# Kernel optimization log

Measured on AMD Instinct MI355X. Metric: run time of the kernel, lower is better.

The kernel has to match this reference:

```python
import jax, jax.numpy as jnp
import numpy as np

# Hardware-emulation constants (from init_kwargs, NeuroSim-style QLinear)
WL_IN = 8        # input activation bit width (bit-serial)
WL_W = 8         # weight bit width
CELL_BIT = 2     # bits per memory cell -> 4 weight slices
SUB = 128        # crossbar sub-array size (rows summed in analog)
ADC_BITS = 5     # ADC precision per partial sum
ONOFF = 10.0     # cell on/off conductance ratio
VARI = 0.05      # multiplicative device variation sigma


def _adc_quant(x, bits, axes):
    # LinearQuantizeOut: uniform quantization between tensor min/max
    mn = jnp.min(x, axis=axes, keepdims=True)
    mx = jnp.max(x, axis=axes, keepdims=True)
    step = (mx - mn) * (2.0 ** (-bits))
    step = jnp.where(step <= 0, 1.0, step)
    idx = jnp.clip(jnp.floor((x - mn) / step), 0.0, 2.0 ** bits - 1.0)
    return idx * step + mn


def _qlinear_hw(x, w, noise):
    """Analog PIM crossbar emulation of y = x @ w.T with bit-serial inputs,
    bit-sliced cells, on/off-ratio offset + dummy column, device variation,
    per-subarray ADC quantization."""
    B, N = x.shape
    F = w.shape[0]
    I, W, K = WL_IN, WL_W, WL_W // CELL_BIT
    cr = 2.0 ** CELL_BIT
    lower, upper = 1.0 / ONOFF, 1.0
    S = (N + SUB - 1) // SUB
    Np = S * SUB
    # quantize input to I bits in [0,1]; weight to W-bit integer in [0, 2^W-1]
    xq = jnp.round(jnp.clip(x, 0.0, 1.0) * (2.0 ** I - 1.0))            # [B, N]
    Xi = jnp.clip(jnp.round((w + 1.0) * 0.5 * (2.0 ** W - 1.0)), 0.0, 2.0 ** W - 1.0)  # [F, N]
    xq = jnp.pad(xq, ((0, 0), (0, Np - N)))
    Xi = jnp.pad(Xi, ((0, 0), (0, Np - N)))
    zpow = 2.0 ** jnp.arange(I, dtype=x.dtype)
    kpow = cr ** jnp.arange(K, dtype=x.dtype)
    bits = jnp.mod(jnp.floor(xq[..., None] / zpow), 2.0)                # [B, Np, I]
    slc = jnp.mod(jnp.floor(Xi[..., None] / kpow), cr)                  # [F, Np, K]
    g = slc * (upper - lower) + (cr - 1.0) * lower                      # cell conductances
    g = g * (1.0 + VARI * noise)                                        # device variation
    bits = bits.reshape(B, S, SUB, I)
    g = g.reshape(F, S, SUB, K)
    # analog partial sums per (input bit i, subarray s, weight slice k)
    P = jnp.einsum('bsai,fsak->iskbf', bits, g)                         # [I,S,K,B,F]
    # dummy column (all cells at lowest conductance), identical across F
    D = jnp.transpose(bits.sum(axis=2), (2, 1, 0)) * ((cr - 1.0) * lower)  # [I,S,B]
    Pq = _adc_quant(P, ADC_BITS, axes=(3, 4))
    Dq = _adc_quant(D, ADC_BITS, axes=(2,))
    scal = (2.0 ** jnp.arange(I, dtype=x.dtype))[:, None] * (cr ** jnp.arange(K, dtype=x.dtype))[None, :]
    acc = jnp.einsum('iskbf,ik->bf', Pq - Dq[:, :, None, :, None], scal) / (upper - lower)
    # undo integer mappings: w = 2*Xi/(2^W-1) - 1, x = xq/(2^I-1)
    out = 2.0 * acc / ((2.0 ** I - 1.0) * (2.0 ** W - 1.0)) \
          - xq.sum(axis=1, keepdims=True) / (2.0 ** I - 1.0)
    return out


def _qlinear(x, w, noise):
    # straight-through quantized weight (WAGE-style STE) + hardware forward
    Xi = jnp.clip(jnp.round((w + 1.0) * 0.5 * (2.0 ** WL_W - 1.0)), 0.0, 2.0 ** WL_W - 1.0)
    wq = 2.0 * Xi / (2.0 ** WL_W - 1.0) - 1.0
    wq_ste = w + jax.lax.stop_gradient(wq - w)
    out_ideal = x @ wq_ste.T
    out_hw = _qlinear_hw(x, w, noise)
    return out_ideal + jax.lax.stop_gradient(out_hw - out_ideal)


def setup_inputs() -> dict:
    key = jax.random.key(0)
    k1, k2, k3, k4, k5 = jax.random.split(key, 5)
    x = jax.random.uniform(k1, (1024, 784), dtype=jnp.float32)
    w1 = jax.random.normal(k2, (512, 784), dtype=jnp.float32) * 0.05
    w3 = jax.random.normal(k3, (10, 512), dtype=jnp.float32) * 0.08
    noise1 = jax.random.normal(k4, (512, 896, 4), dtype=jnp.float32)  # 784 padded to 7*128
    noise3 = jax.random.normal(k5, (10, 512, 4), dtype=jnp.float32)   # 512 = 4*128 exact
    return {"x": x, "w1": w1, "w3": w3, "noise1": noise1, "noise3": noise3}


def reference(x, w1, w3, noise1, noise3):
    h = jnp.tanh(_qlinear(x, w1, noise1))   # QLinear(784,512) + Tanh
    return _qlinear(h, w3, noise3)          # QLinear(512,10)
```

## Files before the change

### kernel.cpp

```cpp
#include <hip/hip_runtime.h>

#define FLTMAX 3.402823466e+38f


__global__ void prep1_kernel(const float* __restrict__ x, float* __restrict__ xq1,
                             float* __restrict__ sx1, unsigned* __restrict__ stats1)
{
    __shared__ float red[128];
    int b = blockIdx.x;
    if (blockIdx.x == 0) {
        for (int t = threadIdx.x; t < 224; t += 128) {
            stats1[t * 2] = 0x7F7FFFFFu; stats1[t * 2 + 1] = 0u;
        }
    }
    float psum = 0.f;
    for (int n = threadIdx.x; n < 896; n += 128) {
        float v = 0.f;
        if (n < 784) {
            float xv = x[b * 784 + n];
            xv = fminf(fmaxf(xv, 0.f), 1.f);
            v = rintf(__fmul_rn(xv, 255.f));
        }
        xq1[b * 896 + n] = v;
        psum += v;
    }
    red[threadIdx.x] = psum;
    __syncthreads();
    for (int w = 64; w >= 1; w >>= 1) {
        if (threadIdx.x < w) red[threadIdx.x] += red[threadIdx.x + w];
        __syncthreads();
    }
    if (threadIdx.x == 0) sx1[b] = red[0];
}

__global__ void bitpack_kernel(const float* __restrict__ xq1, unsigned* __restrict__ xqb)
{
    int gid = blockIdx.x * 256 + threadIdx.x;
    if (gid >= 1024 * 28) return;
    int b = gid / 28, w = gid % 28;
    unsigned words[8] = {0, 0, 0, 0, 0, 0, 0, 0};
    const float* src = &xq1[b * 896 + w * 32];
#pragma unroll 8
    for (int n = 0; n < 32; ++n) {
        int v = (int)src[n];
#pragma unroll
        for (int i = 0; i < 8; ++i) words[i] |= ((unsigned)((v >> i) & 1)) << n;
    }
#pragma unroll
    for (int i = 0; i < 8; ++i) xqb[(i * 1024 + b) * 28 + w] = words[i];
}

__global__ void prepg1t_kernel(const float* __restrict__ w1, const float* __restrict__ noise1,
                               float* __restrict__ g1t)
{
    __shared__ float t[4][32][33];
    const int n0 = blockIdx.x * 32, f0 = blockIdx.y * 32;
    const int tid = threadIdx.x;
    {
        int n = tid & 31, fi = tid >> 5;
#pragma unroll
        for (int p = 0; p < 4; ++p) {
            int f = p * 8 + fi;
            int gn = n0 + n, gf = f0 + f;
            float gv[4] = {0.f, 0.f, 0.f, 0.f};
            if (gn < 784) {
                float w = w1[gf * 784 + gn];
                float Xi = fminf(fmaxf(rintf(__fmul_rn(__fmul_rn(__fadd_rn(w, 1.f), 0.5f), 255.f)),
                                       0.f), 255.f);
                int xi = (int)Xi;
                float4 nz = *(const float4*)&noise1[(gf * 896 + gn) * 4];
                float nzv[4] = {nz.x, nz.y, nz.z, nz.w};
#pragma unroll
                for (int k = 0; k < 4; ++k) {
                    int slc = (xi >> (2 * k)) & 3;
                    float base = __fadd_rn(__fmul_rn((float)slc, 0.9f), 0.3f);
                    float nf = __fadd_rn(1.f, __fmul_rn(0.05f, nzv[k]));
                    gv[k] = __fmul_rn(base, nf);
                }
            }
#pragma unroll
            for (int k = 0; k < 4; ++k) t[k][n][f] = gv[k];
        }
    }
    __syncthreads();
    {
        int f = tid & 31, nn = tid >> 5;
#pragma unroll
        for (int p = 0; p < 4; ++p) {
            int n = p * 8 + nn;
#pragma unroll
            for (int k = 0; k < 4; ++k)
                g1t[(n0 + n) * 2048 + k * 512 + f0 + f] = t[k][n][f];
        }
    }
}

__global__ void prepg2_kernel(const float* __restrict__ w3, const float* __restrict__ noise3,
                              float* __restrict__ g2t)
{
    int gid = blockIdx.x * 256 + threadIdx.x;
    if (gid >= 10 * 512) return;
    int f = gid / 512, n = gid % 512;
    float w = w3[f * 512 + n];
    float Xi = fminf(fmaxf(rintf(__fmul_rn(__fmul_rn(__fadd_rn(w, 1.f), 0.5f), 255.f)),
                           0.f), 255.f);
    int xi = (int)Xi;
#pragma unroll
    for (int k = 0; k < 4; ++k) {
        int slc = (xi >> (2 * k)) & 3;
        float base = __fadd_rn(__fmul_rn((float)slc, 0.9f), 0.3f);
        float nf = __fadd_rn(1.f, __fmul_rn(0.05f, noise3[(f * 512 + n) * 4 + k]));
        g2t[n * 40 + k * 10 + f] = __fmul_rn(base, nf);
    }
}

__global__ void dqpop_kernel(const unsigned* __restrict__ xqb, float* __restrict__ Dq,
                             int S, int wpr)
{
    __shared__ float red[512];
    const int i = blockIdx.x / S, s = blockIdx.x % S;
    const int tid = threadIdx.x;
    float D[4];
    float mn = FLTMAX, mx = -FLTMAX;
#pragma unroll
    for (int u = 0; u < 4; ++u) {
        int b = tid + u * 256;
        uint4 w = *(const uint4*)&xqb[(i * 1024 + b) * wpr + s * 4];
        int c = __popc(w.x) + __popc(w.y) + __popc(w.z) + __popc(w.w);
        D[u] = __fmul_rn((float)c, 0.3f);
        mn = fminf(mn, D[u]);
        mx = fmaxf(mx, D[u]);
    }
    red[tid] = mn; red[256 + tid] = mx;
    __syncthreads();
    for (int w = 128; w >= 1; w >>= 1) {
        if (tid < w) {
            red[tid] = fminf(red[tid], red[tid + w]);
            red[256 + tid] = fmaxf(red[256 + tid], red[256 + tid + w]);
        }
        __syncthreads();
    }
    mn = red[0]; mx = red[256];
    float step = __fmul_rn(__fsub_rn(mx, mn), 0.03125f);
    if (step <= 0.f) step = 1.f;
#pragma unroll
    for (int u = 0; u < 4; ++u) {
        int b = tid + u * 256;
        float idx = fminf(fmaxf(floorf(__fdiv_rn(__fsub_rn(D[u], mn), step)), 0.f), 31.f);
        Dq[(i * S + s) * 1024 + b] = __fadd_rn(__fmul_rn(idx, step), mn);
    }
}

__global__ void dterm_kernel(const float* __restrict__ Dq, float* __restrict__ dterm, int S)
{
    int b = blockIdx.x * 256 + threadIdx.x;
    if (b >= 1024) return;
    float sum = 0.f;
    for (int i = 0; i < 8; ++i) {
        float sc = (float)(85 << i);
        for (int s = 0; s < S; ++s) sum = fmaf(Dq[(i * S + s) * 1024 + b], sc, sum);
    }
    dterm[b] = sum;
}

#define BK 32
__global__ __launch_bounds__(256, 4) void mm1_kernel(
    const unsigned* __restrict__ xqb, const float* __restrict__ g1t,
    float* __restrict__ P, unsigned* __restrict__ stats, int s0)
{
    __shared__ __align__(16) float Bs[BK][132];
    __shared__ unsigned Abits[128];
    __shared__ float red[512];
    const int tid = threadIdx.x;
    const int sl = blockIdx.x >> 6;
    const int r = blockIdx.x & 63;
    const int i = r >> 3;
    const int b0 = (r & 7) * 128;
    const int s = s0 + sl;
    const int colBase = blockIdx.y * 128;
    const int tx = tid & 15, ty = tid >> 4;

    const int aB = tid >> 5;
    const int eB = (tid & 31) << 2;

    float4 pB[4];
    unsigned pAw = 0;
#pragma unroll
    for (int u = 0; u < 4; ++u)
        pB[u] = *(const float4*)&g1t[(s * 128 + u * 8 + aB) * 2048 + colBase + eB];
    if (tid < 128) pAw = xqb[(i * 1024 + b0 + tid) * 28 + s * 4];

    float acc[8][8] = {};

    for (int ac = 0; ac < 4; ++ac) {
        __syncthreads();
#pragma unroll
        for (int u = 0; u < 4; ++u)
            *(float4*)&Bs[u * 8 + aB][eB] = pB[u];
        if (tid < 128) Abits[tid] = pAw;
        __syncthreads();

        if (ac < 3) {
            const int n0 = s * 128 + (ac + 1) * BK;
#pragma unroll
            for (int u = 0; u < 4; ++u)
                pB[u] = *(const float4*)&g1t[(n0 + u * 8 + aB) * 2048 + colBase + eB];
            if (tid < 128) pAw = xqb[(i * 1024 + b0 + tid) * 28 + s * 4 + ac + 1];
        }

        unsigned wrd[8];
#pragma unroll
        for (int u = 0; u < 4; ++u) {
            wrd[u]     = Abits[(ty << 2) + u];
            wrd[4 + u] = Abits[64 + (ty << 2) + u];
        }

#pragma unroll 4
        for (int a = 0; a < BK; ++a) {
            float br[8];
            *(float4*)&br[0] = *(const float4*)&Bs[a][(tx << 2)];
            *(float4*)&br[4] = *(const float4*)&Bs[a][64 + (tx << 2)];
#pragma unroll
            for (int u = 0; u < 8; ++u) {
                float ab = (float)((wrd[u] >> a) & 1u);
#pragma unroll
                for (int v = 0; v < 8; ++v)
                    acc[u][v] = fmaf(ab, br[v], acc[u][v]);
            }
        }
    }

#pragma unroll
    for (int uh = 0; uh < 2; ++uh)
#pragma unroll
        for (int u = 0; u < 4; ++u) {
            int row = (sl * 8 + i) * 1024 + b0 + uh * 64 + (ty << 2) + u;
#pragma unroll
            for (int vh = 0; vh < 2; ++vh) {
                float4 v = make_float4(acc[uh * 4 + u][vh * 4 + 0], acc[uh * 4 + u][vh * 4 + 1],
                                       acc[uh * 4 + u][vh * 4 + 2], acc[uh * 4 + u][vh * 4 + 3]);
                *(float4*)&P[(size_t)row * 2048 + colBase + vh * 64 + (tx << 2)] = v;
            }
        }

    float mn = acc[0][0], mx = acc[0][0];
#pragma unroll
    for (int u = 0; u < 8; ++u)
#pragma unroll
        for (int v = 0; v < 8; ++v) { mn = fminf(mn, acc[u][v]); mx = fmaxf(mx, acc[u][v]); }
    red[tid] = mn; red[256 + tid] = mx;
    __syncthreads();
    for (int w = 128; w >= 1; w >>= 1) {
        if (tid < w) {
            red[tid] = fminf(red[tid], red[tid + w]);
            red[256 + tid] = fmaxf(red[256 + tid], red[256 + tid + w]);
        }
        __syncthreads();
    }
    if (tid == 0) {
        int k = colBase >> 9;
        int slot = ((s * 8 + i) * 4 + k) * 2;
        atomicMin(&stats[slot], __float_as_uint(red[0]));
        atomicMax(&stats[slot + 1], __float_as_uint(red[256]));
    }
}

__global__ void quant1_kernel(const float* __restrict__ P, const unsigned* __restrict__ stats,
                              float* __restrict__ acc1, int s0, int G, int first)
{
    int gid = blockIdx.x * 256 + threadIdx.x;
    int b = gid >> 7, f4 = gid & 127;
    float4 accR;
    if (first) accR = make_float4(0.f, 0.f, 0.f, 0.f);
    else       accR = *(const float4*)&acc1[(b << 9) + (f4 << 2)];
    for (int sl = 0; sl < G; ++sl) {
        int s = s0 + sl;
        float4 sum = make_float4(0.f, 0.f, 0.f, 0.f);
        for (int i = 0; i < 8; ++i) {
#pragma unroll
            for (int k = 0; k < 4; ++k) {
                int slot = ((s * 8 + i) * 4 + k) * 2;
                float mn = __uint_as_float(stats[slot]);
                float mx = __uint_as_float(stats[slot + 1]);
                float step = __fmul_rn(__fsub_rn(mx, mn), 0.03125f);
                if (step <= 0.f) step = 1.f;
                float4 val = *(const float4*)&P[(size_t)((sl * 8 + i) * 1024 + b) * 2048
                                                + (k << 9) + (f4 << 2)];
                float sc = (float)(1 << (i + 2 * k));
                float ix, pq;
                ix = fminf(fmaxf(floorf(__fdiv_rn(__fsub_rn(val.x, mn), step)), 0.f), 31.f);
                pq = __fadd_rn(__fmul_rn(ix, step), mn); sum.x = fmaf(pq, sc, sum.x);
                ix = fminf(fmaxf(floorf(__fdiv_rn(__fsub_rn(val.y, mn), step)), 0.f), 31.f);
                pq = __fadd_rn(__fmul_rn(ix, step), mn); sum.y = fmaf(pq, sc, sum.y);
                ix = fminf(fmaxf(floorf(__fdiv_rn(__fsub_rn(val.z, mn), step)), 0.f), 31.f);
                pq = __fadd_rn(__fmul_rn(ix, step), mn); sum.z = fmaf(pq, sc, sum.z);
                ix = fminf(fmaxf(floorf(__fdiv_rn(__fsub_rn(val.w, mn), step)), 0.f), 31.f);
                pq = __fadd_rn(__fmul_rn(ix, step), mn); sum.w = fmaf(pq, sc, sum.w);
            }
        }
        accR.x = __fadd_rn(accR.x, sum.x);
        accR.y = __fadd_rn(accR.y, sum.y);
        accR.z = __fadd_rn(accR.z, sum.z);
        accR.w = __fadd_rn(accR.w, sum.w);
    }
    *(float4*)&acc1[(b << 9) + (f4 << 2)] = accR;
}

__global__ void finish1_kernel(const float* __restrict__ acc1, const float* __restrict__ dterm1,
                               const float* __restrict__ sx1, float* __restrict__ xq2,
                               unsigned* __restrict__ xqb2)
{
    int gid = blockIdx.x * 256 + threadIdx.x;
    int b = gid >> 9, f = gid & 511;
    float total = __fsub_rn(acc1[gid], dterm1[b]);
    float acc = __fdiv_rn(total, 0.9f);
    float o = __fsub_rn(__fdiv_rn(__fmul_rn(2.f, acc), 65025.f), __fdiv_rn(sx1[b], 255.f));
    float h = tanhf(o);
    h = fminf(fmaxf(h, 0.f), 1.f);
    float code = rintf(__fmul_rn(h, 255.f));
    xq2[gid] = code;
    int ci = (int)code;
    int lane = threadIdx.x & 63;
#pragma unroll
    for (int i = 0; i < 8; ++i) {
        unsigned long long m = __ballot((ci >> i) & 1);
        if ((lane & 31) == 0) {
            unsigned wv = (lane & 32) ? (unsigned)(m >> 32) : (unsigned)m;
            xqb2[(i * 1024 + b) * 16 + (f >> 5)] = wv;
        }
    }
}

__global__ void sx2_kernel(const float* __restrict__ xq2, float* __restrict__ sx2)
{
    __shared__ float red[128];
    int b = blockIdx.x;
    float psum = 0.f;
    for (int n = threadIdx.x; n < 512; n += 128) psum += xq2[b * 512 + n];
    red[threadIdx.x] = psum;
    __syncthreads();
    for (int w = 64; w >= 1; w >>= 1) {
        if (threadIdx.x < w) red[threadIdx.x] += red[threadIdx.x + w];
        __syncthreads();
    }
    if (threadIdx.x == 0) sx2[b] = red[0];
}

__global__ void mm2_kernel(const float* __restrict__ xq2, const float* __restrict__ g2t,
                           float* __restrict__ P2)
{
    int gid = blockIdx.x * 256 + threadIdx.x;
    if (gid >= 40960) return;
    int f = gid % 10;
    int b = (gid / 10) & 1023;
    int s = gid / 10240;
    float acc[8][4] = {};
    for (int a = 0; a < 128; ++a) {
        int n = s * 128 + a;
        int xi = (int)xq2[b * 512 + n];
        float g0 = g2t[n * 40 + f];
        float gA = g2t[n * 40 + 10 + f];
        float gB = g2t[n * 40 + 20 + f];
        float gC = g2t[n * 40 + 30 + f];
#pragma unroll
        for (int i = 0; i < 8; ++i) {
            float bi = (float)((xi >> i) & 1);
            acc[i][0] = fmaf(bi, g0, acc[i][0]);
            acc[i][1] = fmaf(bi, gA, acc[i][1]);
            acc[i][2] = fmaf(bi, gB, acc[i][2]);
            acc[i][3] = fmaf(bi, gC, acc[i][3]);
        }
    }
#pragma unroll
    for (int i = 0; i < 8; ++i)
#pragma unroll
        for (int k = 0; k < 4; ++k)
            P2[(size_t)((s * 8 + i) * 4 + k) * 10240 + b * 10 + f] = acc[i][k];
}

__global__ void stat2_kernel(const float* __restrict__ P2, float2* __restrict__ stats2)
{
    __shared__ float red[512];
    int p = blockIdx.x;
    int tid = threadIdx.x;
    float mn = FLTMAX, mx = -FLTMAX;
    for (int t = tid; t < 10240; t += 256) {
        float v = P2[(size_t)p * 10240 + t];
        mn = fminf(mn, v); mx = fmaxf(mx, v);
    }
    red[tid] = mn; red[256 + tid] = mx;
    __syncthreads();
    for (int w = 128; w >= 1; w >>= 1) {
        if (tid < w) {
            red[tid] = fminf(red[tid], red[tid + w]);
            red[256 + tid] = fmaxf(red[256 + tid], red[256 + tid + w]);
        }
        __syncthreads();
    }
    if (tid == 0) {
        float step = __fmul_rn(__fsub_rn(red[256], red[0]), 0.03125f);
        if (step <= 0.f) step = 1.f;
        stats2[p] = make_float2(red[0], step);
    }
}

__global__ void out2_kernel(const float* __restrict__ P2, const float2* __restrict__ stats2,
                            const float* __restrict__ dterm2, const float* __restrict__ sx2,
                            float* __restrict__ out)
{
    int gid = blockIdx.x * 256 + threadIdx.x;
    if (gid >= 10240) return;
    int b = gid / 10;
    float sum = 0.f;
    for (int s = 0; s < 4; ++s)
        for (int i = 0; i < 8; ++i)
#pragma unroll
            for (int k = 0; k < 4; ++k) {
                int p = (s * 8 + i) * 4 + k;
                float2 st = stats2[p];
                float val = P2[(size_t)p * 10240 + gid];
                float idx = fminf(fmaxf(floorf(__fdiv_rn(__fsub_rn(val, st.x), st.y)), 0.f), 31.f);
                float pq = __fadd_rn(__fmul_rn(idx, st.y), st.x);
                sum = fmaf(pq, (float)(1 << (i + 2 * k)), sum);
            }
    float total = __fsub_rn(sum, dterm2[b]);
    float acc = __fdiv_rn(total, 0.9f);
    out[gid] = __fsub_rn(__fdiv_rn(__fmul_rn(2.f, acc), 65025.f), __fdiv_rn(sx2[b], 255.f));
}

extern "C" void kernel_launch(void* const* d_in, const int* in_sizes, int n_in,
                              void* d_out, int out_size, void* d_ws, size_t ws_size,
                              hipStream_t stream)
{
    const float* x      = (const float*)d_in[0];
    const float* w1     = (const float*)d_in[1];
    const float* w3     = (const float*)d_in[2];
    const float* noise1 = (const float*)d_in[3];
    const float* noise3 = (const float*)d_in[4];
    float* out = (float*)d_out;
    float* ws  = (float*)d_ws;

    float*    xq1    = ws + 0;
    float*    g1t    = ws + 917504;
    float*    acc1   = ws + 2752512;
    float*    xq2    = ws + 3276800;
    float*    P2     = ws + 3801088;
    float*    g2t    = ws + 5111808;
    float*    Dq1    = ws + 5132288;
    float*    Dq2    = ws + 5189632;
    float*    sx1    = ws + 5222400;
    float*    sx2    = ws + 5223424;
    float*    dterm1 = ws + 5224448;
    float*    dterm2 = ws + 5225472;
    float2*   stats2 = (float2*)(ws + 5226496);
    unsigned* stats1 = (unsigned*)(ws + 5226752);
    unsigned* xqb    = (unsigned*)(ws + 5227264);
    unsigned* xqb2   = (unsigned*)(ws + 5456640);
    float*    Ps     = ws + 5587712;

    const size_t fixedf = 5587712;
    const size_t planef = 16777216;
    int G = 1;
    while (G < 7 && (fixedf + (size_t)(G + 1) * planef) * sizeof(float) <= ws_size) ++G;

    prep1_kernel<<<1024, 128, 0, stream>>>(x, xq1, sx1, stats1);
    prepg1t_kernel<<<dim3(28, 16), 256, 0, stream>>>(w1, noise1, g1t);
    bitpack_kernel<<<112, 256, 0, stream>>>(xq1, xqb);
    dqpop_kernel<<<56, 256, 0, stream>>>(xqb, Dq1, 7, 28);
    dterm_kernel<<<4, 256, 0, stream>>>(Dq1, dterm1, 7);

    for (int s0 = 0; s0 < 7; s0 += G) {
        int Gc = (7 - s0 < G) ? (7 - s0) : G;
        mm1_kernel<<<dim3(Gc * 64, 16), 256, 0, stream>>>(xqb, g1t, Ps, stats1, s0);
        quant1_kernel<<<512, 256, 0, stream>>>(Ps, stats1, acc1, s0, Gc, s0 == 0);
    }

    finish1_kernel<<<2048, 256, 0, stream>>>(acc1, dterm1, sx1, xq2, xqb2);
    sx2_kernel<<<1024, 128, 0, stream>>>(xq2, sx2);
    prepg2_kernel<<<20, 256, 0, stream>>>(w3, noise3, g2t);
    dqpop_kernel<<<32, 256, 0, stream>>>(xqb2, Dq2, 4, 16);
    dterm_kernel<<<4, 256, 0, stream>>>(Dq2, dterm2, 4);
    mm2_kernel<<<160, 256, 0, stream>>>(xq2, g2t, P2);
    stat2_kernel<<<128, 256, 0, stream>>>(P2, stats2);
    out2_kernel<<<40, 256, 0, stream>>>(P2, stats2, dterm2, sx2, out);
}
```

Measured before the change: 668.1 us.

## Fuse layer-1 crossbar matmul and ADC quantization into one cooperative kernel

Replaces the per-subarray mm1 + quant1 kernel pairs with a single cooperative kernel. Partial sums stay in registers, the per-(s,i,k) min/max is reduced with atomics, and a grid-wide sync separates the reduction from quantizing in place. This removes the large partial-sum plane writes and reads to global memory and the repeated launches. In exchange it adds 14 grid syncs, relies on all 512 blocks being co-resident, and changes the bit-pack layout to a transposed form for coalesced loads.

```diff
diff --git a/kernel.cpp b/kernel.cpp
--- a/kernel.cpp
+++ b/kernel.cpp
@@ -1,4 +1,7 @@
 #include <hip/hip_runtime.h>
+#include <hip/hip_cooperative_groups.h>
+
+namespace cg = cooperative_groups;
 
 #define FLTMAX 3.402823466e+38f
 
@@ -33,11 +36,11 @@
     if (threadIdx.x == 0) sx1[b] = red[0];
 }
 
-__global__ void bitpack_kernel(const float* __restrict__ xq1, unsigned* __restrict__ xqb)
+__global__ void bitpackT_kernel(const float* __restrict__ xq1, unsigned* __restrict__ xqbT)
 {
     int gid = blockIdx.x * 256 + threadIdx.x;
-    if (gid >= 1024 * 28) return;
-    int b = gid / 28, w = gid % 28;
+    if (gid >= 28672) return;
+    int w = gid >> 10, b = gid & 1023;
     unsigned words[8] = {0, 0, 0, 0, 0, 0, 0, 0};
     const float* src = &xq1[b * 896 + w * 32];
 #pragma unroll 8
@@ -47,7 +50,7 @@
         for (int i = 0; i < 8; ++i) words[i] |= ((unsigned)((v >> i) & 1)) << n;
     }
 #pragma unroll
-    for (int i = 0; i < 8; ++i) xqb[(i * 1024 + b) * 28 + w] = words[i];
+    for (int i = 0; i < 8; ++i) xqbT[(i * 28 + w) * 1024 + b] = words[i];
 }
 
 __global__ void prepg1t_kernel(const float* __restrict__ w1, const float* __restrict__ noise1,
@@ -114,6 +117,44 @@
     }
 }
 
+__global__ void dqpopT_kernel(const unsigned* __restrict__ xqbT, float* __restrict__ Dq)
+{
+    __shared__ float red[512];
+    const int i = blockIdx.x / 7, s = blockIdx.x % 7;
+    const int tid = threadIdx.x;
+    float D[4];
+    float mn = FLTMAX, mx = -FLTMAX;
+#pragma unroll
+    for (int u = 0; u < 4; ++u) {
+        int b = tid + u * 256;
+        int c = 0;
+#pragma unroll
+        for (int w = 0; w < 4; ++w)
+            c += __popc(xqbT[(i * 28 + s * 4 + w) * 1024 + b]);
+        D[u] = __fmul_rn((float)c, 0.3f);
+        mn = fminf(mn, D[u]);
+        mx = fmaxf(mx, D[u]);
+    }
+    red[tid] = mn; red[256 + tid] = mx;
+    __syncthreads();
+    for (int w = 128; w >= 1; w >>= 1) {
+        if (tid < w) {
+            red[tid] = fminf(red[tid], red[tid + w]);
+            red[256 + tid] = fmaxf(red[256 + tid], red[256 + tid + w]);
+        }
+        __syncthreads();
+    }
+    mn = red[0]; mx = red[256];
+    float step = __fmul_rn(__fsub_rn(mx, mn), 0.03125f);
+    if (step <= 0.f) step = 1.f;
+#pragma unroll
+    for (int u = 0; u < 4; ++u) {
+        int b = tid + u * 256;
+        float idx = fminf(fmaxf(floorf(__fdiv_rn(__fsub_rn(D[u], mn), step)), 0.f), 31.f);
+        Dq[(i * 7 + s) * 1024 + b] = __fadd_rn(__fmul_rn(idx, step), mn);
+    }
+}
+
 __global__ void dqpop_kernel(const unsigned* __restrict__ xqb, float* __restrict__ Dq,
                              int S, int wpr)
 {
@@ -163,147 +204,134 @@
     dterm[b] = sum;
 }
 
-#define BK 32
-__global__ __launch_bounds__(256, 4) void mm1_kernel(
-    const unsigned* __restrict__ xqb, const float* __restrict__ g1t,
-    float* __restrict__ P, unsigned* __restrict__ stats, int s0)
-{
-    __shared__ __align__(16) float Bs[BK][132];
-    __shared__ unsigned Abits[128];
-    __shared__ float red[512];
+__global__ __launch_bounds__(256, 2) void coop_mm1(
+    const unsigned* __restrict__ xqbT, const float* __restrict__ g1t,
+    unsigned* __restrict__ stats, float* __restrict__ acc1)
+{
+    cg::grid_group gridg = cg::this_grid();
+    __shared__ __align__(16) float Bs[4][128][16];
+    __shared__ unsigned Aw[8][4][64];
+    __shared__ float wredmn[16][4], wredmx[16][4];
+    __shared__ float stf[16][2];
     const int tid = threadIdx.x;
-    const int sl = blockIdx.x >> 6;
-    const int r = blockIdx.x & 63;
-    const int i = r >> 3;
-    const int b0 = (r & 7) * 128;
-    const int s = s0 + sl;
-    const int colBase = blockIdx.y * 128;
-    const int tx = tid & 15, ty = tid >> 4;
-
-    const int aB = tid >> 5;
-    const int eB = (tid & 31) << 2;
-
-    float4 pB[4];
-    unsigned pAw = 0;
-#pragma unroll
-    for (int u = 0; u < 4; ++u)
-        pB[u] = *(const float4*)&g1t[(s * 128 + u * 8 + aB) * 2048 + colBase + eB];
-    if (tid < 128) pAw = xqb[(i * 1024 + b0 + tid) * 28 + s * 4];
-
-    float acc[8][8] = {};
-
-    for (int ac = 0; ac < 4; ++ac) {
-        __syncthreads();
-#pragma unroll
-        for (int u = 0; u < 4; ++u)
-            *(float4*)&Bs[u * 8 + aB][eB] = pB[u];
-        if (tid < 128) Abits[tid] = pAw;
-        __syncthreads();
-
-        if (ac < 3) {
-            const int n0 = s * 128 + (ac + 1) * BK;
-#pragma unroll
-            for (int u = 0; u < 4; ++u)
-                pB[u] = *(const float4*)&g1t[(n0 + u * 8 + aB) * 2048 + colBase + eB];
-            if (tid < 128) pAw = xqb[(i * 1024 + b0 + tid) * 28 + s * 4 + ac + 1];
-        }
-
-        unsigned wrd[8];
-#pragma unroll
-        for (int u = 0; u < 4; ++u) {
-            wrd[u]     = Abits[(ty << 2) + u];
-            wrd[4 + u] = Abits[64 + (ty << 2) + u];
-        }
-
+    const int b0 = (blockIdx.x >> 5) * 64;
+    const int f0 = (blockIdx.x & 31) * 16;
+    const int lane = tid & 63;
+    const int wv = tid >> 6;
+    const int b = b0 + lane;
+
+    float accR[4] = {0.f, 0.f, 0.f, 0.f};
+
+    for (int s = 0; s < 7; ++s) {
+        __syncthreads();
+#pragma unroll
+        for (int u = 0; u < 8; ++u) {
+            int idx = u * 256 + tid;
+            int k = idx >> 9, a = (idx >> 2) & 127, fg = idx & 3;
+            *(float4*)&Bs[k][a][fg * 4] =
+                *(const float4*)&g1t[(s * 128 + a) * 2048 + k * 512 + f0 + fg * 4];
+            int i = idx >> 8, w = (idx >> 6) & 3, bb = idx & 63;
+            Aw[i][w][bb] = xqbT[(i * 28 + s * 4 + w) * 1024 + b0 + bb];
+        }
+        __syncthreads();
+
+        float sum[4] = {0.f, 0.f, 0.f, 0.f};
+        for (int half = 0; half < 2; ++half) {
+            float acc[4][4][4] = {};
+            for (int w = 0; w < 4; ++w) {
+                unsigned myw[4];
+#pragma unroll
+                for (int il = 0; il < 4; ++il) myw[il] = Aw[half * 4 + il][w][lane];
 #pragma unroll 4
-        for (int a = 0; a < BK; ++a) {
-            float br[8];
-            *(float4*)&br[0] = *(const float4*)&Bs[a][(tx << 2)];
-            *(float4*)&br[4] = *(const float4*)&Bs[a][64 + (tx << 2)];
-#pragma unroll
-            for (int u = 0; u < 8; ++u) {
-                float ab = (float)((wrd[u] >> a) & 1u);
-#pragma unroll
-                for (int v = 0; v < 8; ++v)
-                    acc[u][v] = fmaf(ab, br[v], acc[u][v]);
+                for (int bit = 0; bit < 32; ++bit) {
+                    int a = w * 32 + bit;
+                    float4 br0 = *(const float4*)&Bs[0][a][wv * 4];
+                    float4 br1 = *(const float4*)&Bs[1][a][wv * 4];
+                    float4 br2 = *(const float4*)&Bs[2][a][wv * 4];
+                    float4 br3 = *(const float4*)&Bs[3][a][wv * 4];
+#pragma unroll
+                    for (int il = 0; il < 4; ++il) {
+                        float ab = (float)((myw[il] >> bit) & 1u);
+                        acc[il][0][0] = fmaf(ab, br0.x, acc[il][0][0]);
+                        acc[il][0][1] = fmaf(ab, br0.y, acc[il][0][1]);
+                        acc[il][0][2] = fmaf(ab, br0.z, acc[il][0][2]);
+                        acc[il][0][3] = fmaf(ab, br0.w, acc[il][0][3]);
+                        acc[il][1][0] = fmaf(ab, br1.x, acc[il][1][0]);
+                        acc[il][1][1] = fmaf(ab, br1.y, acc[il][1][1]);
+                        acc[il][1][2] = fmaf(ab, br1.z, acc[il][1][2]);
+                        acc[il][1][3] = fmaf(ab, br1.w, acc[il][1][3]);
+                        acc[il][2][0] = fmaf(ab, br2.x, acc[il][2][0]);
+                        acc[il][2][1] = fmaf(ab, br2.y, acc[il][2][1]);
+                        acc[il][2][2] = fmaf(ab, br2.z, acc[il][2][2]);
+                        acc[il][2][3] = fmaf(ab, br2.w, acc[il][2][3]);
+                        acc[il][3][0] = fmaf(ab, br3.x, acc[il][3][0]);
+                        acc[il][3][1] = fmaf(ab, br3.y, acc[il][3][1]);
+                        acc[il][3][2] = fmaf(ab, br3.z, acc[il][3][2]);
+                        acc[il][3][3] = fmaf(ab, br3.w, acc[il][3][3]);
+                    }
+                }
             }
-        }
-    }
-
-#pragma unroll
-    for (int uh = 0; uh < 2; ++uh)
-#pragma unroll
-        for (int u = 0; u < 4; ++u) {
-            int row = (sl * 8 + i) * 1024 + b0 + uh * 64 + (ty << 2) + u;
-#pragma unroll
-            for (int vh = 0; vh < 2; ++vh) {
-                float4 v = make_float4(acc[uh * 4 + u][vh * 4 + 0], acc[uh * 4 + u][vh * 4 + 1],
-                                       acc[uh * 4 + u][vh * 4 + 2], acc[uh * 4 + u][vh * 4 + 3]);
-                *(float4*)&P[(size_t)row * 2048 + colBase + vh * 64 + (tx << 2)] = v;
+#pragma unroll
+            for (int il = 0; il < 4; ++il)
+#pragma unroll
+                for (int k = 0; k < 4; ++k) {
+                    float mn = fminf(fminf(acc[il][k][0], acc[il][k][1]),
+                                     fminf(acc[il][k][2], acc[il][k][3]));
+                    float mx = fmaxf(fmaxf(acc[il][k][0], acc[il][k][1]),
+                                     fmaxf(acc[il][k][2], acc[il][k][3]));
+                    for (int off = 32; off >= 1; off >>= 1) {
+                        mn = fminf(mn, __shfl_xor(mn, off, 64));
+                        mx = fmaxf(mx, __shfl_xor(mx, off, 64));
+                    }
+                    if (lane == 0) { wredmn[il * 4 + k][wv] = mn; wredmx[il * 4 + k][wv] = mx; }
+                }
+            __syncthreads();
+            if (tid < 16) {
+                float mn = fminf(fminf(wredmn[tid][0], wredmn[tid][1]),
+                                 fminf(wredmn[tid][2], wredmn[tid][3]));
+                float mx = fmaxf(fmaxf(wredmx[tid][0], wredmx[tid][1]),
+                                 fmaxf(wredmx[tid][2], wredmx[tid][3]));
+                int i = half * 4 + (tid >> 2), k = tid & 3;
+                int slot = ((s * 8 + i) * 4 + k) * 2;
+                atomicMin(&stats[slot], __float_as_uint(mn));
+                atomicMax(&stats[slot + 1], __float_as_uint(mx));
             }
-        }
-
-    float mn = acc[0][0], mx = acc[0][0];
-#pragma unroll
-    for (int u = 0; u < 8; ++u)
-#pragma unroll
-        for (int v = 0; v < 8; ++v) { mn = fminf(mn, acc[u][v]); mx = fmaxf(mx, acc[u][v]); }
-    red[tid] = mn; red[256 + tid] = mx;
-    __syncthreads();
-    for (int w = 128; w >= 1; w >>= 1) {
-        if (tid < w) {
-            red[tid] = fminf(red[tid], red[tid + w]);
-            red[256 + tid] = fmaxf(red[256 + tid], red[256 + tid + w]);
-        }
-        __syncthreads();
-    }
-    if (tid == 0) {
-        int k = colBase >> 9;
-        int slot = ((s * 8 + i) * 4 + k) * 2;
-        atomicMin(&stats[slot], __float_as_uint(red[0]));
-        atomicMax(&stats[slot + 1], __float_as_uint(red[256]));
-    }
-}
-
-__global__ void quant1_kernel(const float* __restrict__ P, const unsigned* __restrict__ stats,
-                              float* __restrict__ acc1, int s0, int G, int first)
-{
-    int gid = blockIdx.x * 256 + threadIdx.x;
-    int b = gid >> 7, f4 = gid & 127;
-    float4 accR;
-    if (first) accR = make_float4(0.f, 0.f, 0.f, 0.f);
-    else       accR = *(const float4*)&acc1[(b << 9) + (f4 << 2)];
-    for (int sl = 0; sl < G; ++sl) {
-        int s = s0 + sl;
-        float4 sum = make_float4(0.f, 0.f, 0.f, 0.f);
-        for (int i = 0; i < 8; ++i) {
-#pragma unroll
-            for (int k = 0; k < 4; ++k) {
+            __threadfence();
+            gridg.sync();
+            if (tid < 16) {
+                int i = half * 4 + (tid >> 2), k = tid & 3;
                 int slot = ((s * 8 + i) * 4 + k) * 2;
-                float mn = __uint_as_float(stats[slot]);
-                float mx = __uint_as_float(stats[slot + 1]);
+                unsigned umn = atomicOr(&stats[slot], 0u);
+                unsigned umx = atomicOr(&stats[slot + 1], 0u);
+                float mn = __uint_as_float(umn), mx = __uint_as_float(umx);
                 float step = __fmul_rn(__fsub_rn(mx, mn), 0.03125f);
                 if (step <= 0.f) step = 1.f;
-                float4 val = *(const float4*)&P[(size_t)((sl * 8 + i) * 1024 + b) * 2048
-                                                + (k << 9) + (f4 << 2)];
-                float sc = (float)(1 << (i + 2 * k));
-                float ix, pq;
-                ix = fminf(fmaxf(floorf(__fdiv_rn(__fsub_rn(val.x, mn), step)), 0.f), 31.f);
-                pq = __fadd_rn(__fmul_rn(ix, step), mn); sum.x = fmaf(pq, sc, sum.x);
-                ix = fminf(fmaxf(floorf(__fdiv_rn(__fsub_rn(val.y, mn), step)), 0.f), 31.f);
-                pq = __fadd_rn(__fmul_rn(ix, step), mn); sum.y = fmaf(pq, sc, sum.y);
-                ix = fminf(fmaxf(floorf(__fdiv_rn(__fsub_rn(val.z, mn), step)), 0.f), 31.f);
-                pq = __fadd_rn(__fmul_rn(ix, step), mn); sum.z = fmaf(pq, sc, sum.z);
-                ix = fminf(fmaxf(floorf(__fdiv_rn(__fsub_rn(val.w, mn), step)), 0.f), 31.f);
-                pq = __fadd_rn(__fmul_rn(ix, step), mn); sum.w = fmaf(pq, sc, sum.w);
+                stf[tid][0] = mn; stf[tid][1] = step;
             }
-        }
-        accR.x = __fadd_rn(accR.x, sum.x);
-        accR.y = __fadd_rn(accR.y, sum.y);
-        accR.z = __fadd_rn(accR.z, sum.z);
-        accR.w = __fadd_rn(accR.w, sum.w);
-    }
-    *(float4*)&acc1[(b << 9) + (f4 << 2)] = accR;
+            __syncthreads();
+#pragma unroll
+            for (int il = 0; il < 4; ++il) {
+                int i = half * 4 + il;
+#pragma unroll
+                for (int k = 0; k < 4; ++k) {
+                    float mn = stf[il * 4 + k][0], step = stf[il * 4 + k][1];
+                    float sc = (float)(1 << (i + 2 * k));
+#pragma unroll
+                    for (int j = 0; j < 4; ++j) {
+                        float ix = fminf(fmaxf(floorf(__fdiv_rn(__fsub_rn(acc[il][k][j], mn),
+                                                                step)), 0.f), 31.f);
+                        float pq = __fadd_rn(__fmul_rn(ix, step), mn);
+                        sum[j] = fmaf(pq, sc, sum[j]);
+                    }
+                }
+            }
+        }
+#pragma unroll
+        for (int j = 0; j < 4; ++j) accR[j] = __fadd_rn(accR[j], sum[j]);
+    }
+
+    *(float4*)&acc1[b * 512 + f0 + wv * 4] =
+        make_float4(accR[0], accR[1], accR[2], accR[3]);
 }
 
 __global__ void finish1_kernel(const float* __restrict__ acc1, const float* __restrict__ dterm1,
@@ -454,25 +482,19 @@
     float*    dterm2 = ws + 5225472;
     float2*   stats2 = (float2*)(ws + 5226496);
     unsigned* stats1 = (unsigned*)(ws + 5226752);
-    unsigned* xqb    = (unsigned*)(ws + 5227264);
+    unsigned* xqbT   = (unsigned*)(ws + 5227264);
     unsigned* xqb2   = (unsigned*)(ws + 5456640);
-    float*    Ps     = ws + 5587712;
-
-    const size_t fixedf = 5587712;
-    const size_t planef = 16777216;
-    int G = 1;
-    while (G < 7 && (fixedf + (size_t)(G + 1) * planef) * sizeof(float) <= ws_size) ++G;
 
     prep1_kernel<<<1024, 128, 0, stream>>>(x, xq1, sx1, stats1);
+    bitpackT_kernel<<<112, 256, 0, stream>>>(xq1, xqbT);
     prepg1t_kernel<<<dim3(28, 16), 256, 0, stream>>>(w1, noise1, g1t);
-    bitpack_kernel<<<112, 256, 0, stream>>>(xq1, xqb);
-    dqpop_kernel<<<56, 256, 0, stream>>>(xqb, Dq1, 7, 28);
+    dqpopT_kernel<<<56, 256, 0, stream>>>(xqbT, Dq1);
     dterm_kernel<<<4, 256, 0, stream>>>(Dq1, dterm1, 7);
 
-    for (int s0 = 0; s0 < 7; s0 += G) {
-        int Gc = (7 - s0 < G) ? (7 - s0) : G;
-        mm1_kernel<<<dim3(Gc * 64, 16), 256, 0, stream>>>(xqb, g1t, Ps, stats1, s0);
-        quant1_kernel<<<512, 256, 0, stream>>>(Ps, stats1, acc1, s0, Gc, s0 == 0);
+    {
+        void* args[] = {(void*)&xqbT, (void*)&g1t, (void*)&stats1, (void*)&acc1};
+        hipLaunchCooperativeKernel((const void*)coop_mm1, dim3(512), dim3(256),
+                                   args, 0, stream);
     }
 
     finish1_kernel<<<2048, 256, 0, stream>>>(acc1, dterm1, sx1, xq2, xqb2);
```

Measured after the change: 1.709 ms. 156% more time.

## Fuse bitpacking and sx2 reductions, transpose bit layout, cap plane grouping

Applied to the files above, without the earlier changes.

Bit-packing moves into prep1, working from shared memory, so the intermediate xq1 buffer and one kernel launch go away. The packed bits are stored transposed (word-major, batch-contiguous), which makes the per-row loads in mm1 and the new dqpopT kernel coalesced. The sx2 row sum is folded into finish1, which now launches one 512-thread block per row. The subarray group size G is capped at 2 instead of growing up to 7. That means more mm1/quant1 passes, but each partial-sum plane working set is smaller and more likely to stay in cache.

```diff
diff --git a/kernel.cpp b/kernel.cpp
--- a/kernel.cpp
+++ b/kernel.cpp
@@ -3,12 +3,13 @@
 #define FLTMAX 3.402823466e+38f
 
 
-__global__ void prep1_kernel(const float* __restrict__ x, float* __restrict__ xq1,
-                             float* __restrict__ sx1, unsigned* __restrict__ stats1)
-{
+__global__ void prep1_kernel(const float* __restrict__ x, float* __restrict__ sx1,
+                             unsigned* __restrict__ xqbT, unsigned* __restrict__ stats1)
+{
+    __shared__ float xr[896];
     __shared__ float red[128];
     int b = blockIdx.x;
-    if (blockIdx.x == 0) {
+    if (b == 0) {
         for (int t = threadIdx.x; t < 224; t += 128) {
             stats1[t * 2] = 0x7F7FFFFFu; stats1[t * 2 + 1] = 0u;
         }
@@ -21,7 +22,7 @@
             xv = fminf(fmaxf(xv, 0.f), 1.f);
             v = rintf(__fmul_rn(xv, 255.f));
         }
-        xq1[b * 896 + n] = v;
+        xr[n] = v;
         psum += v;
     }
     red[threadIdx.x] = psum;
@@ -31,23 +32,18 @@
         __syncthreads();
     }
     if (threadIdx.x == 0) sx1[b] = red[0];
-}
-
-__global__ void bitpack_kernel(const float* __restrict__ xq1, unsigned* __restrict__ xqb)
-{
-    int gid = blockIdx.x * 256 + threadIdx.x;
-    if (gid >= 1024 * 28) return;
-    int b = gid / 28, w = gid % 28;
-    unsigned words[8] = {0, 0, 0, 0, 0, 0, 0, 0};
-    const float* src = &xq1[b * 896 + w * 32];
+    if (threadIdx.x < 28) {
+        int w = threadIdx.x;
+        unsigned words[8] = {0, 0, 0, 0, 0, 0, 0, 0};
 #pragma unroll 8
-    for (int n = 0; n < 32; ++n) {
-        int v = (int)src[n];
-#pragma unroll
-        for (int i = 0; i < 8; ++i) words[i] |= ((unsigned)((v >> i) & 1)) << n;
-    }
-#pragma unroll
-    for (int i = 0; i < 8; ++i) xqb[(i * 1024 + b) * 28 + w] = words[i];
+        for (int n = 0; n < 32; ++n) {
+            int v = (int)xr[w * 32 + n];
+#pragma unroll
+            for (int i = 0; i < 8; ++i) words[i] |= ((unsigned)((v >> i) & 1)) << n;
+        }
+#pragma unroll
+        for (int i = 0; i < 8; ++i) xqbT[(i * 28 + w) * 1024 + b] = words[i];
+    }
 }
 
 __global__ void prepg1t_kernel(const float* __restrict__ w1, const float* __restrict__ noise1,
@@ -114,6 +110,44 @@
     }
 }
 
+__global__ void dqpopT_kernel(const unsigned* __restrict__ xqbT, float* __restrict__ Dq)
+{
+    __shared__ float red[512];
+    const int i = blockIdx.x / 7, s = blockIdx.x % 7;
+    const int tid = threadIdx.x;
+    float D[4];
+    float mn = FLTMAX, mx = -FLTMAX;
+#pragma unroll
+    for (int u = 0; u < 4; ++u) {
+        int b = tid + u * 256;
+        int c = 0;
+#pragma unroll
+        for (int w = 0; w < 4; ++w)
+            c += __popc(xqbT[(i * 28 + s * 4 + w) * 1024 + b]);
+        D[u] = __fmul_rn((float)c, 0.3f);
+        mn = fminf(mn, D[u]);
+        mx = fmaxf(mx, D[u]);
+    }
+    red[tid] = mn; red[256 + tid] = mx;
+    __syncthreads();
+    for (int w = 128; w >= 1; w >>= 1) {
+        if (tid < w) {
+            red[tid] = fminf(red[tid], red[tid + w]);
+            red[256 + tid] = fmaxf(red[256 + tid], red[256 + tid + w]);
+        }
+        __syncthreads();
+    }
+    mn = red[0]; mx = red[256];
+    float step = __fmul_rn(__fsub_rn(mx, mn), 0.03125f);
+    if (step <= 0.f) step = 1.f;
+#pragma unroll
+    for (int u = 0; u < 4; ++u) {
+        int b = tid + u * 256;
+        float idx = fminf(fmaxf(floorf(__fdiv_rn(__fsub_rn(D[u], mn), step)), 0.f), 31.f);
+        Dq[(i * 7 + s) * 1024 + b] = __fadd_rn(__fmul_rn(idx, step), mn);
+    }
+}
+
 __global__ void dqpop_kernel(const unsigned* __restrict__ xqb, float* __restrict__ Dq,
                              int S, int wpr)
 {
@@ -165,7 +199,7 @@
 
 #define BK 32
 __global__ __launch_bounds__(256, 4) void mm1_kernel(
-    const unsigned* __restrict__ xqb, const float* __restrict__ g1t,
+    const unsigned* __restrict__ xqbT, const float* __restrict__ g1t,
     float* __restrict__ P, unsigned* __restrict__ stats, int s0)
 {
     __shared__ __align__(16) float Bs[BK][132];
@@ -188,7 +222,7 @@
 #pragma unroll
     for (int u = 0; u < 4; ++u)
         pB[u] = *(const float4*)&g1t[(s * 128 + u * 8 + aB) * 2048 + colBase + eB];
-    if (tid < 128) pAw = xqb[(i * 1024 + b0 + tid) * 28 + s * 4];
+    if (tid < 128) pAw = xqbT[(i * 28 + s * 4) * 1024 + b0 + tid];
 
     float acc[8][8] = {};
 
@@ -205,7 +239,7 @@
 #pragma unroll
             for (int u = 0; u < 4; ++u)
                 pB[u] = *(const float4*)&g1t[(n0 + u * 8 + aB) * 2048 + colBase + eB];
-            if (tid < 128) pAw = xqb[(i * 1024 + b0 + tid) * 28 + s * 4 + ac + 1];
+            if (tid < 128) pAw = xqbT[(i * 28 + s * 4 + ac + 1) * 1024 + b0 + tid];
         }
 
         unsigned wrd[8];
@@ -308,10 +342,12 @@
 
 __global__ void finish1_kernel(const float* __restrict__ acc1, const float* __restrict__ dterm1,
                                const float* __restrict__ sx1, float* __restrict__ xq2,
-                               unsigned* __restrict__ xqb2)
-{
-    int gid = blockIdx.x * 256 + threadIdx.x;
-    int b = gid >> 9, f = gid & 511;
+                               unsigned* __restrict__ xqb2, float* __restrict__ sx2)
+{
+    __shared__ float red[512];
+    int b = blockIdx.x;
+    int f = threadIdx.x;
+    int gid = b * 512 + f;
     float total = __fsub_rn(acc1[gid], dterm1[b]);
     float acc = __fdiv_rn(total, 0.9f);
     float o = __fsub_rn(__fdiv_rn(__fmul_rn(2.f, acc), 65025.f), __fdiv_rn(sx1[b], 255.f));
@@ -320,7 +356,7 @@
     float code = rintf(__fmul_rn(h, 255.f));
     xq2[gid] = code;
     int ci = (int)code;
-    int lane = threadIdx.x & 63;
+    int lane = f & 63;
 #pragma unroll
     for (int i = 0; i < 8; ++i) {
         unsigned long long m = __ballot((ci >> i) & 1);
@@ -329,21 +365,13 @@
             xqb2[(i * 1024 + b) * 16 + (f >> 5)] = wv;
         }
     }
-}
-
-__global__ void sx2_kernel(const float* __restrict__ xq2, float* __restrict__ sx2)
-{
-    __shared__ float red[128];
-    int b = blockIdx.x;
-    float psum = 0.f;
-    for (int n = threadIdx.x; n < 512; n += 128) psum += xq2[b * 512 + n];
-    red[threadIdx.x] = psum;
-    __syncthreads();
-    for (int w = 64; w >= 1; w >>= 1) {
-        if (threadIdx.x < w) red[threadIdx.x] += red[threadIdx.x + w];
-        __syncthreads();
-    }
-    if (threadIdx.x == 0) sx2[b] = red[0];
+    red[f] = code;
+    __syncthreads();
+    for (int w = 256; w >= 1; w >>= 1) {
+        if (f < w) red[f] += red[f + w];
+        __syncthreads();
+    }
+    if (f == 0) sx2[b] = red[0];
 }
 
 __global__ void mm2_kernel(const float* __restrict__ xq2, const float* __restrict__ g2t,
@@ -440,43 +468,39 @@
     float* out = (float*)d_out;
     float* ws  = (float*)d_ws;
 
-    float*    xq1    = ws + 0;
-    float*    g1t    = ws + 917504;
-    float*    acc1   = ws + 2752512;
-    float*    xq2    = ws + 3276800;
-    float*    P2     = ws + 3801088;
-    float*    g2t    = ws + 5111808;
-    float*    Dq1    = ws + 5132288;
-    float*    Dq2    = ws + 5189632;
-    float*    sx1    = ws + 5222400;
-    float*    sx2    = ws + 5223424;
-    float*    dterm1 = ws + 5224448;
-    float*    dterm2 = ws + 5225472;
-    float2*   stats2 = (float2*)(ws + 5226496);
-    unsigned* stats1 = (unsigned*)(ws + 5226752);
-    unsigned* xqb    = (unsigned*)(ws + 5227264);
-    unsigned* xqb2   = (unsigned*)(ws + 5456640);
-    float*    Ps     = ws + 5587712;
-
-    const size_t fixedf = 5587712;
+    float*    g1t    = ws + 0;
+    float*    acc1   = ws + 1835008;
+    float*    xq2    = ws + 2359296;
+    float*    P2     = ws + 2883584;
+    float*    g2t    = ws + 4194304;
+    float*    Dq1    = ws + 4214784;
+    float*    Dq2    = ws + 4272128;
+    float*    sx1    = ws + 4304896;
+    float*    sx2    = ws + 4305920;
+    float*    dterm1 = ws + 4306944;
+    float*    dterm2 = ws + 4307968;
+    float2*   stats2 = (float2*)(ws + 4308992);
+    unsigned* stats1 = (unsigned*)(ws + 4309248);
+    unsigned* xqbT   = (unsigned*)(ws + 4309760);
+    unsigned* xqb2   = (unsigned*)(ws + 4539136);
+    float*    Ps     = ws + 4670208;
+
+    const size_t fixedf = 4670208;
     const size_t planef = 16777216;
-    int G = 1;
-    while (G < 7 && (fixedf + (size_t)(G + 1) * planef) * sizeof(float) <= ws_size) ++G;
-
-    prep1_kernel<<<1024, 128, 0, stream>>>(x, xq1, sx1, stats1);
+    int G = ((fixedf + 2 * planef) * sizeof(float) <= ws_size) ? 2 : 1;
+
+    prep1_kernel<<<1024, 128, 0, stream>>>(x, sx1, xqbT, stats1);
     prepg1t_kernel<<<dim3(28, 16), 256, 0, stream>>>(w1, noise1, g1t);
-    bitpack_kernel<<<112, 256, 0, stream>>>(xq1, xqb);
-    dqpop_kernel<<<56, 256, 0, stream>>>(xqb, Dq1, 7, 28);
+    dqpopT_kernel<<<56, 256, 0, stream>>>(xqbT, Dq1);
     dterm_kernel<<<4, 256, 0, stream>>>(Dq1, dterm1, 7);
 
     for (int s0 = 0; s0 < 7; s0 += G) {
         int Gc = (7 - s0 < G) ? (7 - s0) : G;
-        mm1_kernel<<<dim3(Gc * 64, 16), 256, 0, stream>>>(xqb, g1t, Ps, stats1, s0);
+        mm1_kernel<<<dim3(Gc * 64, 16), 256, 0, stream>>>(xqbT, g1t, Ps, stats1, s0);
         quant1_kernel<<<512, 256, 0, stream>>>(Ps, stats1, acc1, s0, Gc, s0 == 0);
     }
 
-    finish1_kernel<<<2048, 256, 0, stream>>>(acc1, dterm1, sx1, xq2, xqb2);
-    sx2_kernel<<<1024, 128, 0, stream>>>(xq2, sx2);
+    finish1_kernel<<<1024, 512, 0, stream>>>(acc1, dterm1, sx1, xq2, xqb2, sx2);
     prepg2_kernel<<<20, 256, 0, stream>>>(w3, noise3, g2t);
     dqpop_kernel<<<32, 256, 0, stream>>>(xqb2, Dq2, 4, 16);
     dterm_kernel<<<4, 256, 0, stream>>>(Dq2, dterm2, 4);
```

Measured after the change: 670.4 us. No clear change (+0.3%).
